# Performance work log

Measured on AMD Instinct MI355X. Metric: run time of the kernel, lower is better.

The kernel has to match this reference:

```python
import jax, jax.numpy as jnp
import numpy as np

N = 38332        # nodes = poi_len - 1 (pinned by fc_layer in_features)
POI_LEN = 38333
CAT_LEN = 400
POI_DIM = 300
CAT_DIM = 100
C = 128          # gcn_channel
L = 5            # gcn_layers
E = 1200000      # edges
NEG = 0.01       # nn.LeakyReLU default slope
GAT_NEG = 0.2    # GATConv attention slope


def _leaky(x, s=NEG):
    return jnp.where(x > 0, x, s * x)


def _gcn_conv(x, W, b, src, dst, ew):
    # PyG GCNConv: self-loops already appended in (src,dst,ew); symmetric norm
    xw = x @ W
    deg = jax.ops.segment_sum(ew, dst, num_segments=N)
    dinv = jnp.where(deg > 0, jax.lax.rsqrt(deg), 0.0)
    norm = dinv[src] * ew * dinv[dst]
    out = jax.ops.segment_sum(xw[src] * norm[:, None], dst, num_segments=N)
    return out + b


def _gat_conv(x, W, a_src, a_dst, b, src, dst):
    # PyG GATConv, 1 head; self-loops already in (src,dst)
    xw = x @ W                      # [N, C]
    al = xw @ a_src                 # [N]
    ar = xw @ a_dst                 # [N]
    e = _leaky(al[src] + ar[dst], GAT_NEG)          # [E+N]
    emax = jax.ops.segment_max(e, dst, num_segments=N)
    ex = jnp.exp(e - emax[dst])
    denom = jax.ops.segment_sum(ex, dst, num_segments=N)
    att = ex / denom[dst]
    out = jax.ops.segment_sum(xw[src] * att[:, None], dst, num_segments=N)
    return out + b


def _graph_norm(x, gamma, beta, alpha, eps=1e-5):
    # PyG GraphNorm over the single graph (all nodes)
    mean = x.mean(0)
    xc = x - alpha * mean
    var = (xc * xc).mean(0)
    return gamma * xc * jax.lax.rsqrt(var + eps) + beta


def _forward(poi_ids, cat_ids, feat3, edge_index, edge_weight, poi_emb, cat_emb,
             Win, b_in, gcn_W, gcn_b, gn_gamma, gn_beta, gn_alpha,
             gat_W, gat_asrc, gat_adst, gat_b, Wout, b_out,
             fc_W1, fc_b1, fc_W2, fc_b2):
    loops = jnp.arange(N, dtype=edge_index.dtype)
    src = jnp.concatenate([edge_index[0], loops])
    dst = jnp.concatenate([edge_index[1], loops])
    ew = jnp.concatenate([edge_weight, jnp.ones((N,), edge_weight.dtype)])
    # node features: [poi_emb | cat_emb | 3 raw floats] -> [N, 403]
    feat = jnp.concatenate([poi_emb[poi_ids], cat_emb[cat_ids], feat3], axis=1)
    x = _leaky(_gcn_conv(feat, Win, b_in, src, dst, ew))
    for l in range(L):  # GcnUnit stack (shared GraphNorm within a unit)
        t = _leaky(_graph_norm(_gcn_conv(x, gcn_W[l], gcn_b[l], src, dst, ew),
                               gn_gamma[l], gn_beta[l], gn_alpha[l]))
        x = x + t
        t = _leaky(_graph_norm(_gat_conv(x, gat_W[l], gat_asrc[l], gat_adst[l], gat_b[l], src, dst),
                               gn_gamma[l], gn_beta[l], gn_alpha[l]))
        x = x + t
    x = _leaky(_gcn_conv(x, Wout, b_out, src, dst, ew)).reshape(-1)  # [N]
    h = jax.nn.relu(x @ fc_W1 + fc_b1)
    return jax.nn.relu(h @ fc_W2 + fc_b2)  # [POI_LEN]


def setup_inputs() -> dict:
    key = jax.random.key(0)
    ks = iter(jax.random.split(key, 24))
    nrm = lambda s, sc=0.05: jax.random.normal(next(ks), s, dtype=jnp.float32) * sc
    return {
        'poi_ids': jax.random.randint(next(ks), (N,), 0, POI_LEN),
        'cat_ids': jax.random.randint(next(ks), (N,), 0, CAT_LEN),
        'feat3': jax.random.normal(next(ks), (N, 3), dtype=jnp.float32),
        'edge_index': jax.random.randint(next(ks), (2, E), 0, N),
        'edge_weight': jax.random.uniform(next(ks), (E,), dtype=jnp.float32),
        'poi_emb': nrm((POI_LEN, POI_DIM)),
        'cat_emb': nrm((CAT_LEN, CAT_DIM)),
        'Win': nrm((POI_DIM + CAT_DIM + 3, C)),
        'b_in': jnp.zeros((C,), jnp.float32),
        'gcn_W': nrm((L, C, C)),
        'gcn_b': jnp.zeros((L, C), jnp.float32),
        'gn_gamma': jnp.ones((L, C), jnp.float32),
        'gn_beta': jnp.zeros((L, C), jnp.float32),
        'gn_alpha': jnp.ones((L, C), jnp.float32),
        'gat_W': nrm((L, C, C)),
        'gat_asrc': nrm((L, C)),
        'gat_adst': nrm((L, C)),
        'gat_b': jnp.zeros((L, C), jnp.float32),
        'Wout': nrm((C, 1)),
        'b_out': jnp.zeros((1,), jnp.float32),
        'fc_W1': nrm((N, 128)),
        'fc_b1': jnp.zeros((128,), jnp.float32),
        'fc_W2': nrm((128, POI_LEN)),
        'fc_b2': jnp.zeros((POI_LEN,), jnp.float32),
    }


def reference(poi_ids, cat_ids, feat3, edge_index, edge_weight, poi_emb, cat_emb,
              Win, b_in, gcn_W, gcn_b, gn_gamma, gn_beta, gn_alpha,
              gat_W, gat_asrc, gat_adst, gat_b, Wout, b_out,
              fc_W1, fc_b1, fc_W2, fc_b2):
    return _forward(poi_ids, cat_ids, feat3, edge_index, edge_weight, poi_emb, cat_emb,
                    Win, b_in, gcn_W, gcn_b, gn_gamma, gn_beta, gn_alpha,
                    gat_W, gat_asrc, gat_adst, gat_b, Wout, b_out,
                    fc_W1, fc_b1, fc_W2, fc_b2)
```

## Files before the change

### kernel.cpp

```cpp
#include <hip/hip_runtime.h>

typedef unsigned short ushort_t;
typedef __attribute__((ext_vector_type(8))) short short8v;
typedef __attribute__((ext_vector_type(4))) float floatx4;

__device__ __forceinline__ float b2f(ushort_t u) {
    unsigned int x = ((unsigned int)u) << 16;
    float f; __builtin_memcpy(&f, &x, 4); return f;
}
__device__ __forceinline__ ushort_t f2b(float f) {
    unsigned int x; __builtin_memcpy(&x, &f, 4);
    unsigned int lsb = (x >> 16) & 1u;
    x += 0x7fffu + lsb;
    return (ushort_t)(x >> 16);
}
__device__ __forceinline__ float leaky01(float v) { return v > 0.f ? v : 0.01f * v; }

__global__ void init_k(int* cnt, int N) {
    int i = blockIdx.x * 256 + threadIdx.x;
    if (i < N) cnt[i] = 1;
}

__global__ void count_k(const int* __restrict__ ei, int* cnt, int E) {
    int e = blockIdx.x * 256 + threadIdx.x;
    if (e < E) atomicAdd(&cnt[ei[E + e]], 1);
}

__launch_bounds__(1024)
__global__ void scan_k(const int* __restrict__ cnt, int* rp, int n) {
    __shared__ int wsum[16];
    int tid = threadIdx.x; int lane = tid & 63, wid = tid >> 6;
    int base = 0;
    for (int start = 0; start < n; start += 4096) {
        int v[4]; int s = 0;
        #pragma unroll
        for (int j = 0; j < 4; ++j) {
            int i = start + tid * 4 + j;
            v[j] = (i < n) ? cnt[i] : 0; s += v[j];
        }
        int sc = s;
        #pragma unroll
        for (int off = 1; off < 64; off <<= 1) {
            int t = __shfl_up(sc, off);
            if (lane >= off) sc += t;
        }
        if (lane == 63) wsum[wid] = sc;
        __syncthreads();
        if (wid == 0) {
            int ws = (lane < 16) ? wsum[lane] : 0;
            #pragma unroll
            for (int off = 1; off < 16; off <<= 1) {
                int t = __shfl_up(ws, off);
                if (lane >= off) ws += t;
            }
            if (lane < 16) wsum[lane] = ws;
        }
        __syncthreads();
        int wbase = (wid > 0) ? wsum[wid - 1] : 0;
        int excl = base + wbase + (sc - s);
        #pragma unroll
        for (int j = 0; j < 4; ++j) {
            int i = start + tid * 4 + j;
            if (i < n) rp[i] = excl;
            excl += v[j];
        }
        int total = wsum[15];
        __syncthreads();
        base += total;
    }
    if (tid == 0) rp[n] = base;
}

__global__ void post_k(const int* __restrict__ rp, int* fill, float2* er, int N) {
    int i = blockIdx.x * 256 + threadIdx.x;
    if (i < N) {
        int p = rp[i];
        fill[i] = p + 1;
        er[p] = make_float2(__int_as_float(i), 1.0f);
    }
}

__global__ void scat_k(const int* __restrict__ ei, const float* __restrict__ ew,
                       int* fill, float2* er, int E) {
    int e = blockIdx.x * 256 + threadIdx.x;
    if (e < E) {
        int dst = ei[E + e];
        int pos = atomicAdd(&fill[dst], 1);
        er[pos] = make_float2(__int_as_float(ei[e]), ew[e]);
    }
}

__global__ void deg_k(const int* __restrict__ rp, const float2* __restrict__ er,
                      float* dinv, int N) {
    int wave = threadIdx.x >> 6, lane = threadIdx.x & 63;
    int node = blockIdx.x * 4 + wave;
    if (node >= N) return;
    int s0 = rp[node], end = rp[node + 1];
    float sum = 0.f;
    for (int s = s0 + lane; s < end; s += 64) sum += er[s].y;
    #pragma unroll
    for (int off = 32; off; off >>= 1) sum += __shfl_xor(sum, off);
    if (lane == 0) dinv[node] = rsqrtf(sum);
}

__global__ void coef_k(const int* __restrict__ rp, float2* er,
                       const float* __restrict__ dinv, int N) {
    int wave = threadIdx.x >> 6, lane = threadIdx.x & 63;
    int node = blockIdx.x * 4 + wave;
    if (node >= N) return;
    int s0 = rp[node], end = rp[node + 1];
    float di = dinv[node];
    for (int s = s0 + lane; s < end; s += 64) {
        float2 r = er[s];
        int src = __float_as_int(r.x);
        r.y = dinv[src] * r.y * di;
        er[s] = r;
    }
}

__global__ void prep_w(const float* __restrict__ gcn_W, const float* __restrict__ gat_W,
                       const float* __restrict__ Win, ushort_t* __restrict__ wt,
                       ushort_t* __restrict__ wtin) {
    int idx = blockIdx.x * 256 + threadIdx.x;
    if (idx < 10 * 16384) {
        int l = idx >> 14, r = idx & 16383;
        int n = r >> 7, k = r & 127;
        const float* src = (l < 5) ? (gcn_W + l * 16384) : (gat_W + (l - 5) * 16384);
        wt[idx] = f2b(src[k * 128 + n]);
    } else {
        int idx2 = idx - 10 * 16384;
        if (idx2 < 128 * 320) {
            int n = idx2 / 320, k = idx2 - n * 320;
            wtin[idx2] = f2b(k < 300 ? Win[k * 128 + n] : 0.f);
        }
    }
}

__global__ void cat_proj_k(const float* __restrict__ ce, const float* __restrict__ Win,
                           float* __restrict__ cp) {
    __shared__ float row[100];
    int r = blockIdx.x, tid = threadIdx.x;
    if (tid < 100) row[tid] = ce[r * 100 + tid];
    __syncthreads();
    float acc = 0.f;
    #pragma unroll 4
    for (int k = 0; k < 100; ++k) acc += row[k] * Win[(300 + k) * 128 + tid];
    cp[r * 128 + tid] = acc;
}

__launch_bounds__(256)
__global__ void poi_gemm(const float* __restrict__ pe, const ushort_t* __restrict__ wtin,
                         ushort_t* __restrict__ pp, int P) {
    __shared__ __align__(16) ushort_t As[64 * 328];
    int tid = threadIdx.x;
    int wid = tid >> 6, lane = tid & 63;
    int r0 = blockIdx.x * 64;
    #pragma unroll
    for (int p = 0; p < 80; ++p) {
        int idx = tid + p * 256;
        int row = idx / 320, k = idx - row * 320;
        float v = 0.f;
        if (k < 300 && (r0 + row) < P) v = pe[(size_t)(r0 + row) * 300 + k];
        As[row * 328 + k] = f2b(v);
    }
    __syncthreads();
    int m = lane & 15, q = lane >> 4;
    short8v af[10];
    #pragma unroll
    for (int kc = 0; kc < 10; ++kc)
        af[kc] = *(const short8v*)&As[(wid * 16 + m) * 328 + kc * 32 + q * 8];
    #pragma unroll
    for (int ct = 0; ct < 8; ++ct) {
        const ushort_t* wr = wtin + (size_t)(ct * 16 + m) * 320 + q * 8;
        floatx4 acc = {0.f, 0.f, 0.f, 0.f};
        #pragma unroll
        for (int kc = 0; kc < 10; ++kc) {
            short8v b = *(const short8v*)(wr + kc * 32);
            acc = __builtin_amdgcn_mfma_f32_16x16x32_bf16(af[kc], b, acc, 0, 0, 0);
        }
        int col = ct * 16 + m;
        #pragma unroll
        for (int rg = 0; rg < 4; ++rg) {
            int row = r0 + wid * 16 + q * 4 + rg;
            if (row < P) pp[(size_t)row * 128 + col] = f2b(acc[rg]);
        }
    }
}

__launch_bounds__(256)
__global__ void gemm_mfma(const ushort_t* __restrict__ xb, const ushort_t* __restrict__ wt,
                          ushort_t* __restrict__ xw, int N) {
    __shared__ __align__(16) ushort_t As[64 * 136];
    int tid = threadIdx.x;
    int wid = tid >> 6, lane = tid & 63;
    int r0 = blockIdx.x * 64;
    #pragma unroll
    for (int p = 0; p < 4; ++p) {
        int idx = tid + p * 256;
        int row = idx >> 4, c8 = idx & 15;
        short8v v = *(const short8v*)&xb[(size_t)(r0 + row) * 128 + c8 * 8];
        *(short8v*)&As[row * 136 + c8 * 8] = v;
    }
    __syncthreads();
    int m = lane & 15, q = lane >> 4;
    const int ar = (wid * 16 + m) * 136 + q * 8;
    short8v a0 = *(const short8v*)&As[ar];
    short8v a1 = *(const short8v*)&As[ar + 32];
    short8v a2 = *(const short8v*)&As[ar + 64];
    short8v a3 = *(const short8v*)&As[ar + 96];
    #pragma unroll
    for (int ct = 0; ct < 8; ++ct) {
        const ushort_t* wr = wt + (size_t)(ct * 16 + m) * 128 + q * 8;
        short8v b0 = *(const short8v*)(wr);
        short8v b1 = *(const short8v*)(wr + 32);
        short8v b2 = *(const short8v*)(wr + 64);
        short8v b3 = *(const short8v*)(wr + 96);
        floatx4 acc = {0.f, 0.f, 0.f, 0.f};
        acc = __builtin_amdgcn_mfma_f32_16x16x32_bf16(a0, b0, acc, 0, 0, 0);
        acc = __builtin_amdgcn_mfma_f32_16x16x32_bf16(a1, b1, acc, 0, 0, 0);
        acc = __builtin_amdgcn_mfma_f32_16x16x32_bf16(a2, b2, acc, 0, 0, 0);
        acc = __builtin_amdgcn_mfma_f32_16x16x32_bf16(a3, b3, acc, 0, 0, 0);
        int col = ct * 16 + m;
        #pragma unroll
        for (int rg = 0; rg < 4; ++rg) {
            int row = r0 + wid * 16 + q * 4 + rg;
            if (row < N) xw[(size_t)row * 128 + col] = f2b(acc[rg]);
        }
    }
}

__global__ void combine_k(const ushort_t* __restrict__ pp, const float* __restrict__ cp,
                          const int* __restrict__ poi_ids, const int* __restrict__ cat_ids,
                          const float* __restrict__ feat3, const float* __restrict__ Win,
                          ushort_t* __restrict__ xw, int N) {
    __shared__ float wf0[128], wf1[128], wf2[128];
    int tid = threadIdx.x;
    if (tid < 128) {
        wf0[tid] = Win[400 * 128 + tid];
        wf1[tid] = Win[401 * 128 + tid];
        wf2[tid] = Win[402 * 128 + tid];
    }
    __syncthreads();
    int node = blockIdx.x * 2 + (tid >> 7);
    int c = tid & 127;
    if (node >= N) return;
    int pid = poi_ids[node], cid = cat_ids[node];
    float f0 = feat3[node * 3], f1 = feat3[node * 3 + 1], f2 = feat3[node * 3 + 2];
    float v = b2f(pp[(size_t)pid * 128 + c]) + cp[cid * 128 + c]
            + f0 * wf0[c] + f1 * wf1[c] + f2 * wf2[c];
    xw[(size_t)node * 128 + c] = f2b(v);
}

template <int MODE>
__launch_bounds__(256)
__global__ void agg_k(const ushort_t* __restrict__ xw, const int* __restrict__ rp,
                      const float2* __restrict__ er,
                      const float* __restrict__ al, const float* __restrict__ ar,
                      const float* __restrict__ bias, float* __restrict__ g,
                      ushort_t* __restrict__ xb, int N) {
    int wave = threadIdx.x >> 6, lane = threadIdx.x & 63;
    int node = blockIdx.x * 4 + wave;
    if (node >= N) return;
    int s0 = __builtin_amdgcn_readfirstlane(rp[node]);
    int end = __builtin_amdgcn_readfirstlane(rp[node + 1]);
    float mmax = 0.f, inv = 0.f, ari = 0.f;
    if (MODE == 2) {
        ari = ar[node];
        float mm = -1e30f;
        for (int s = s0 + lane; s < end; s += 64) {
            int src = __float_as_int(er[s].x);
            float e = al[src] + ari; e = e > 0.f ? e : 0.2f * e;
            mm = fmaxf(mm, e);
        }
        #pragma unroll
        for (int off = 32; off; off >>= 1) mm = fmaxf(mm, __shfl_xor(mm, off));
        float ds = 0.f;
        for (int s = s0 + lane; s < end; s += 64) {
            int src = __float_as_int(er[s].x);
            float e = al[src] + ari; e = e > 0.f ? e : 0.2f * e;
            ds += __expf(e - mm);
        }
        #pragma unroll
        for (int off = 32; off; off >>= 1) ds += __shfl_xor(ds, off);
        mmax = mm;
        inv = 1.f / ds;
    }
    int c = lane * 2;
    float ax = 0.f, ay = 0.f;
    int s = s0;
    for (; s + 8 <= end; s += 8) {
        float2 r[8]; ushort2 u[8]; float cf[8];
        #pragma unroll
        for (int j = 0; j < 8; ++j) r[j] = er[s + j];
        #pragma unroll
        for (int j = 0; j < 8; ++j) {
            int src = __float_as_int(r[j].x);
            u[j] = *(const ushort2*)&xw[(size_t)src * 128 + c];
            if (MODE == 2) {
                float e = al[src] + ari; e = e > 0.f ? e : 0.2f * e;
                cf[j] = __expf(e - mmax) * inv;
            } else cf[j] = r[j].y;
        }
        #pragma unroll
        for (int j = 0; j < 8; ++j) {
            ax += cf[j] * b2f(u[j].x);
            ay += cf[j] * b2f(u[j].y);
        }
    }
    for (; s < end; ++s) {
        float2 r = er[s];
        int src = __float_as_int(r.x);
        float cf;
        if (MODE == 2) {
            float e = al[src] + ari; e = e > 0.f ? e : 0.2f * e;
            cf = __expf(e - mmax) * inv;
        } else cf = r.y;
        ushort2 u = *(const ushort2*)&xw[(size_t)src * 128 + c];
        ax += cf * b2f(u.x);
        ay += cf * b2f(u.y);
    }
    float2 b = *(const float2*)&bias[c];
    ax += b.x; ay += b.y;
    if (MODE == 1) {
        ax = leaky01(ax); ay = leaky01(ay);
        float2 o; o.x = ax; o.y = ay;
        *(float2*)&g[(size_t)node * 128 + c] = o;
        ushort2 ub; ub.x = f2b(ax); ub.y = f2b(ay);
        *(ushort2*)&xb[(size_t)node * 128 + c] = ub;
    } else {
        float2 o; o.x = ax; o.y = ay;
        *(float2*)&g[(size_t)node * 128 + c] = o;
    }
}

__global__ void moments_k(const float* __restrict__ g, float* mom, int n32) {
    __shared__ float s1s[256][4], s2s[256][4];
    int tid = threadIdx.x;
    long long T = (long long)gridDim.x * 256;
    float a1[4] = {0.f, 0.f, 0.f, 0.f}, a2[4] = {0.f, 0.f, 0.f, 0.f};
    const float4* g4 = (const float4*)g;
    for (long long idx = (long long)blockIdx.x * 256 + tid; idx < n32; idx += T) {
        float4 v = g4[idx];
        a1[0] += v.x; a2[0] += v.x * v.x;
        a1[1] += v.y; a2[1] += v.y * v.y;
        a1[2] += v.z; a2[2] += v.z * v.z;
        a1[3] += v.w; a2[3] += v.w * v.w;
    }
    #pragma unroll
    for (int j = 0; j < 4; ++j) { s1s[tid][j] = a1[j]; s2s[tid][j] = a2[j]; }
    __syncthreads();
    if (tid < 32) {
        float r1[4] = {0.f, 0.f, 0.f, 0.f}, r2[4] = {0.f, 0.f, 0.f, 0.f};
        for (int t = tid; t < 256; t += 32) {
            #pragma unroll
            for (int j = 0; j < 4; ++j) { r1[j] += s1s[t][j]; r2[j] += s2s[t][j]; }
        }
        #pragma unroll
        for (int j = 0; j < 4; ++j) {
            atomicAdd(&mom[4 * tid + j], r1[j]);
            atomicAdd(&mom[128 + 4 * tid + j], r2[j]);
        }
    }
}

__global__ void normresid_k(float* __restrict__ x, const float* __restrict__ g,
                            const float* __restrict__ mom,
                            const float* __restrict__ gamma, const float* __restrict__ beta,
                            const float* __restrict__ alpha, ushort_t* __restrict__ xb,
                            int n32, int N) {
    __shared__ float sc[128], sh[128];
    int tid = threadIdx.x;
    if (tid < 128) {
        float m = mom[tid] / (float)N;
        float a = alpha[tid];
        float var = mom[128 + tid] / (float)N - 2.f * a * m * m + a * a * m * m;
        float s = gamma[tid] * rsqrtf(var + 1e-5f);
        sc[tid] = s;
        sh[tid] = beta[tid] - s * a * m;
    }
    __syncthreads();
    const float4* g4 = (const float4*)g;
    float4* x4 = (float4*)x;
    ushort4* xb4 = (ushort4*)xb;
    for (long long idx = (long long)blockIdx.x * 256 + tid; idx < n32;
         idx += (long long)gridDim.x * 256) {
        int c0 = (int)((idx * 4) & 127);
        float4 gv = g4[idx];
        float4 xv = x4[idx];
        xv.x += leaky01(sc[c0] * gv.x + sh[c0]);
        xv.y += leaky01(sc[c0 + 1] * gv.y + sh[c0 + 1]);
        xv.z += leaky01(sc[c0 + 2] * gv.z + sh[c0 + 2]);
        xv.w += leaky01(sc[c0 + 3] * gv.w + sh[c0 + 3]);
        x4[idx] = xv;
        ushort4 ub;
        ub.x = f2b(xv.x); ub.y = f2b(xv.y); ub.z = f2b(xv.z); ub.w = f2b(xv.w);
        xb4[idx] = ub;
    }
}

__global__ void alar_k(const ushort_t* __restrict__ xw, const float* __restrict__ asrc,
                       const float* __restrict__ adst, float* al, float* ar, int N) {
    __shared__ float ls[128], ld[128];
    int tid = threadIdx.x;
    if (tid < 128) { ls[tid] = asrc[tid]; ld[tid] = adst[tid]; }
    __syncthreads();
    int i = blockIdx.x * 256 + tid;
    if (i >= N) return;
    const ushort_t* row = xw + (size_t)i * 128;
    float a = 0.f, b = 0.f;
    #pragma unroll 4
    for (int c = 0; c < 128; c += 4) {
        ushort4 u = *(const ushort4*)(row + c);
        float f0 = b2f(u.x), f1 = b2f(u.y), f2 = b2f(u.z), f3 = b2f(u.w);
        a += f0 * ls[c] + f1 * ls[c + 1] + f2 * ls[c + 2] + f3 * ls[c + 3];
        b += f0 * ld[c] + f1 * ld[c + 1] + f2 * ld[c + 2] + f3 * ld[c + 3];
    }
    al[i] = a; ar[i] = b;
}

__global__ void ydot_k(const float* __restrict__ x, const float* __restrict__ Wout,
                       float* yv, int N) {
    __shared__ float w[128];
    int tid = threadIdx.x;
    if (tid < 128) w[tid] = Wout[tid];
    __syncthreads();
    int i = blockIdx.x * 256 + tid;
    if (i >= N) return;
    const float* row = x + (size_t)i * 128;
    float acc = 0.f;
    #pragma unroll 4
    for (int c = 0; c < 128; c += 4) {
        float4 v = *(const float4*)(row + c);
        acc += v.x * w[c] + v.y * w[c + 1] + v.z * w[c + 2] + v.w * w[c + 3];
    }
    yv[i] = acc;
}

__global__ void aggs_k(const float* __restrict__ yv, const int* __restrict__ rp,
                       const float2* __restrict__ er,
                       const float* __restrict__ b_out, float* xs, int N) {
    int wave = threadIdx.x >> 6, lane = threadIdx.x & 63;
    int node = blockIdx.x * 4 + wave;
    if (node >= N) return;
    int s0 = rp[node], end = rp[node + 1];
    float acc = 0.f;
    for (int s = s0 + lane; s < end; s += 64) {
        float2 r = er[s];
        acc += r.y * yv[__float_as_int(r.x)];
    }
    #pragma unroll
    for (int off = 32; off; off >>= 1) acc += __shfl_xor(acc, off);
    if (lane == 0) xs[node] = leaky01(acc + b_out[0]);
}

__global__ void fc1_k(const float* __restrict__ xs, const float* __restrict__ W1,
                      float* hacc, int N) {
    __shared__ float sd[256];
    int tid = threadIdx.x;
    int j = tid & 127, half = tid >> 7;
    int r0 = blockIdx.x * 256;
    float acc = 0.f;
    for (int rr = half; rr < 256; rr += 2) {
        int r = r0 + rr;
        if (r < N) acc += xs[r] * W1[(size_t)r * 128 + j];
    }
    sd[tid] = acc;
    __syncthreads();
    if (tid < 128) atomicAdd(&hacc[tid], sd[tid] + sd[tid + 128]);
}

__global__ void fc2_k(const float* __restrict__ hacc, const float* __restrict__ b1,
                      const float* __restrict__ W2, const float* __restrict__ b2v,
                      float* out, int P) {
    __shared__ float hs[128];
    int tid = threadIdx.x;
    if (tid < 128) {
        float h = hacc[tid] + b1[tid];
        hs[tid] = h > 0.f ? h : 0.f;
    }
    __syncthreads();
    int p = blockIdx.x * 256 + tid;
    if (p >= P) return;
    float acc = 0.f;
    #pragma unroll 8
    for (int j = 0; j < 128; ++j) acc += hs[j] * W2[(size_t)j * P + p];
    acc += b2v[p];
    out[p] = acc > 0.f ? acc : 0.f;
}

extern "C" void kernel_launch(void* const* d_in, const int* in_sizes, int n_in,
                              void* d_out, int out_size, void* d_ws, size_t ws_size,
                              hipStream_t stream) {
    const int*   poi_ids  = (const int*)d_in[0];
    const int*   cat_ids  = (const int*)d_in[1];
    const float* feat3    = (const float*)d_in[2];
    const int*   ei       = (const int*)d_in[3];
    const float* ew       = (const float*)d_in[4];
    const float* poi_emb  = (const float*)d_in[5];
    const float* cat_emb  = (const float*)d_in[6];
    const float* Win      = (const float*)d_in[7];
    const float* b_in     = (const float*)d_in[8];
    const float* gcn_W    = (const float*)d_in[9];
    const float* gcn_b    = (const float*)d_in[10];
    const float* gn_gamma = (const float*)d_in[11];
    const float* gn_beta  = (const float*)d_in[12];
    const float* gn_alpha = (const float*)d_in[13];
    const float* gat_W    = (const float*)d_in[14];
    const float* gat_asrc = (const float*)d_in[15];
    const float* gat_adst = (const float*)d_in[16];
    const float* gat_b    = (const float*)d_in[17];
    const float* Wout     = (const float*)d_in[18];
    const float* b_out    = (const float*)d_in[19];
    const float* fc_W1    = (const float*)d_in[20];
    const float* fc_b1    = (const float*)d_in[21];
    const float* fc_W2    = (const float*)d_in[22];
    const float* fc_b2    = (const float*)d_in[23];

    const int N = in_sizes[0];
    const int E = in_sizes[4];
    const int POI = in_sizes[5] / 300;
    const int P = out_size;
    const int TOT = E + N;
    const int n128 = N * 128;
    const int n32 = n128 / 4;
    const int NPAD = ((N + 63) / 64) * 64;
    const int PPAD = ((POI + 63) / 64) * 64;

    char* w = (char*)d_ws;
    size_t off = 0;
    auto take = [&](size_t bytes) -> char* {
        char* p = w + off;
        off = (off + bytes + 255) & ~(size_t)255;
        return p;
    };
    float*    x    = (float*)take((size_t)n128 * 4);
    float*    g    = (float*)take((size_t)n128 * 4);
    ushort_t* xb   = (ushort_t*)take((size_t)NPAD * 128 * 2);
    ushort_t* xw   = (ushort_t*)take((size_t)NPAD * 128 * 2);
    ushort_t* pp   = (ushort_t*)take((size_t)PPAD * 128 * 2);
    float*    cp   = (float*)take((size_t)400 * 128 * 4);
    ushort_t* wt   = (ushort_t*)take((size_t)10 * 16384 * 2);
    ushort_t* wtin = (ushort_t*)take((size_t)128 * 320 * 2);
    int*    rp   = (int*)take((size_t)(N + 1) * 4);
    int*    cnt  = (int*)take((size_t)N * 4);
    int*    fill = (int*)take((size_t)N * 4);
    float*  dinv = (float*)take((size_t)N * 4);
    float2* er   = (float2*)take((size_t)TOT * 8);
    float*  al   = (float*)take((size_t)N * 4);
    float*  ar   = (float*)take((size_t)N * 4);
    float*  yv   = (float*)take((size_t)N * 4);
    float*  xs   = (float*)take((size_t)N * 4);
    float*  mom  = (float*)take((size_t)(10 * 256 + 128) * 4);
    float*  hacc = mom + 10 * 256;

    const int gN    = (N + 255) / 256;
    const int gE    = (E + 255) / 256;
    const int gMM   = NPAD / 64;
    const int gPOI  = PPAD / 64;
    const int gW    = (N + 3) / 4;
    const int gP    = (P + 255) / 256;

    hipMemsetAsync(mom, 0, (size_t)(10 * 256 + 128) * 4, stream);

    init_k<<<gN, 256, 0, stream>>>(cnt, N);
    count_k<<<gE, 256, 0, stream>>>(ei, cnt, E);
    scan_k<<<1, 1024, 0, stream>>>(cnt, rp, N);
    post_k<<<gN, 256, 0, stream>>>(rp, fill, er, N);
    scat_k<<<gE, 256, 0, stream>>>(ei, ew, fill, er, E);
    deg_k<<<gW, 256, 0, stream>>>(rp, er, dinv, N);
    coef_k<<<gW, 256, 0, stream>>>(rp, er, dinv, N);

    prep_w<<<(10 * 16384 + 128 * 320 + 255) / 256, 256, 0, stream>>>(gcn_W, gat_W, Win, wt, wtin);
    cat_proj_k<<<400, 128, 0, stream>>>(cat_emb, Win, cp);
    poi_gemm<<<gPOI, 256, 0, stream>>>(poi_emb, wtin, pp, POI);
    combine_k<<<(N + 1) / 2, 256, 0, stream>>>(pp, cp, poi_ids, cat_ids, feat3, Win, xw, N);
    agg_k<1><<<gW, 256, 0, stream>>>(xw, rp, er, nullptr, nullptr, b_in, x, xb, N);

    for (int l = 0; l < 5; ++l) {
        gemm_mfma<<<gMM, 256, 0, stream>>>(xb, wt + (size_t)l * 16384, xw, N);
        agg_k<0><<<gW, 256, 0, stream>>>(xw, rp, er, nullptr, nullptr, gcn_b + l * 128, g, nullptr, N);
        moments_k<<<240, 256, 0, stream>>>(g, mom + (2 * l) * 256, n32);
        normresid_k<<<1024, 256, 0, stream>>>(x, g, mom + (2 * l) * 256,
                                              gn_gamma + l * 128, gn_beta + l * 128,
                                              gn_alpha + l * 128, xb, n32, N);
        gemm_mfma<<<gMM, 256, 0, stream>>>(xb, wt + (size_t)(5 + l) * 16384, xw, N);
        alar_k<<<gN, 256, 0, stream>>>(xw, gat_asrc + l * 128, gat_adst + l * 128, al, ar, N);
        agg_k<2><<<gW, 256, 0, stream>>>(xw, rp, er, al, ar, gat_b + l * 128, g, nullptr, N);
        moments_k<<<240, 256, 0, stream>>>(g, mom + (2 * l + 1) * 256, n32);
        normresid_k<<<1024, 256, 0, stream>>>(x, g, mom + (2 * l + 1) * 256,
                                              gn_gamma + l * 128, gn_beta + l * 128,
                                              gn_alpha + l * 128, xb, n32, N);
    }

    ydot_k<<<gN, 256, 0, stream>>>(x, Wout, yv, N);
    aggs_k<<<gW, 256, 0, stream>>>(yv, rp, er, b_out, xs, N);

    fc1_k<<<(N + 255) / 256, 256, 0, stream>>>(xs, fc_W1, hacc, N);
    fc2_k<<<gP, 256, 0, stream>>>(hacc, fc_b1, fc_W2, fc_b2, (float*)d_out, P);
}
```

Measured before the change: 1.581 ms.

## Fuse GraphNorm residual into GEMM, fuse alar into GEMM, restructure aggregation

GraphNorm+residual+bf16 conversion now runs in the GEMM prologue and the attention logits al/ar are computed in the GEMM epilogue, which removes the separate normresid, alar and ydot kernels and the xb buffer. Edge normalization coefficients are computed on the fly from dinv instead of in a coef_k pass. CSR build uses the atomic return position instead of a second atomic fill. Aggregation switches to 8-channel vector loads with 4 edges processed in parallel per wave, followed by cross-lane reductions. The trade-off is extra dinv gathers per edge and a heavier GEMM prologue.

```diff
diff --git a/kernel.cpp b/kernel.cpp
--- a/kernel.cpp
+++ b/kernel.cpp
@@ -21,9 +21,9 @@
     if (i < N) cnt[i] = 1;
 }
 
-__global__ void count_k(const int* __restrict__ ei, int* cnt, int E) {
+__global__ void count_k(const int* __restrict__ ei, int* cnt, int* pos, int E) {
     int e = blockIdx.x * 256 + threadIdx.x;
-    if (e < E) atomicAdd(&cnt[ei[E + e]], 1);
+    if (e < E) pos[e] = atomicAdd(&cnt[ei[E + e]], 1);
 }
 
 __launch_bounds__(1024)
@@ -71,22 +71,18 @@
     if (tid == 0) rp[n] = base;
 }
 
-__global__ void post_k(const int* __restrict__ rp, int* fill, float2* er, int N) {
+__global__ void post_k(const int* __restrict__ rp, float2* er, int N) {
     int i = blockIdx.x * 256 + threadIdx.x;
-    if (i < N) {
-        int p = rp[i];
-        fill[i] = p + 1;
-        er[p] = make_float2(__int_as_float(i), 1.0f);
-    }
+    if (i < N) er[rp[i]] = make_float2(__int_as_float(i), 1.0f);
 }
 
 __global__ void scat_k(const int* __restrict__ ei, const float* __restrict__ ew,
-                       int* fill, float2* er, int E) {
+                       const int* __restrict__ rp, const int* __restrict__ pos,
+                       float2* er, int E) {
     int e = blockIdx.x * 256 + threadIdx.x;
     if (e < E) {
         int dst = ei[E + e];
-        int pos = atomicAdd(&fill[dst], 1);
-        er[pos] = make_float2(__int_as_float(ei[e]), ew[e]);
+        er[rp[dst] + pos[e]] = make_float2(__int_as_float(ei[e]), ew[e]);
     }
 }
 
@@ -101,21 +97,6 @@
     #pragma unroll
     for (int off = 32; off; off >>= 1) sum += __shfl_xor(sum, off);
     if (lane == 0) dinv[node] = rsqrtf(sum);
-}
-
-__global__ void coef_k(const int* __restrict__ rp, float2* er,
-                       const float* __restrict__ dinv, int N) {
-    int wave = threadIdx.x >> 6, lane = threadIdx.x & 63;
-    int node = blockIdx.x * 4 + wave;
-    if (node >= N) return;
-    int s0 = rp[node], end = rp[node + 1];
-    float di = dinv[node];
-    for (int s = s0 + lane; s < end; s += 64) {
-        float2 r = er[s];
-        int src = __float_as_int(r.x);
-        r.y = dinv[src] * r.y * di;
-        er[s] = r;
-    }
 }
 
 __global__ void prep_w(const float* __restrict__ gcn_W, const float* __restrict__ gat_W,
@@ -187,27 +168,61 @@
     }
 }
 
+template <int NORM, int ALAR>
 __launch_bounds__(256)
-__global__ void gemm_mfma(const ushort_t* __restrict__ xb, const ushort_t* __restrict__ wt,
-                          ushort_t* __restrict__ xw, int N) {
+__global__ void gemm_fused(float* __restrict__ x, const float* __restrict__ gsrc,
+                           const float* __restrict__ mom,
+                           const float* __restrict__ gamma, const float* __restrict__ beta,
+                           const float* __restrict__ alpha,
+                           const ushort_t* __restrict__ wt,
+                           const float* __restrict__ asrc, const float* __restrict__ adst,
+                           ushort_t* __restrict__ xw,
+                           float* __restrict__ al, float* __restrict__ ar, int N) {
     __shared__ __align__(16) ushort_t As[64 * 136];
+    __shared__ float sc[128], sh[128];
     int tid = threadIdx.x;
+    if (NORM) {
+        if (tid < 128) {
+            float mmean = mom[tid] / (float)N;
+            float a = alpha[tid];
+            float var = mom[128 + tid] / (float)N - 2.f * a * mmean * mmean + a * a * mmean * mmean;
+            float s = gamma[tid] * rsqrtf(var + 1e-5f);
+            sc[tid] = s;
+            sh[tid] = beta[tid] - s * a * mmean;
+        }
+        __syncthreads();
+    }
+    int r0 = blockIdx.x * 64;
+    #pragma unroll
+    for (int p = 0; p < 8; ++p) {
+        int idx = tid + p * 256;
+        int row = idx >> 5, c4 = (idx & 31) * 4;
+        int grow = r0 + row;
+        float4 xv = make_float4(0.f, 0.f, 0.f, 0.f);
+        if (grow < N) {
+            xv = *(const float4*)&x[(size_t)grow * 128 + c4];
+            if (NORM) {
+                float4 gv = *(const float4*)&gsrc[(size_t)grow * 128 + c4];
+                xv.x += leaky01(sc[c4] * gv.x + sh[c4]);
+                xv.y += leaky01(sc[c4 + 1] * gv.y + sh[c4 + 1]);
+                xv.z += leaky01(sc[c4 + 2] * gv.z + sh[c4 + 2]);
+                xv.w += leaky01(sc[c4 + 3] * gv.w + sh[c4 + 3]);
+                *(float4*)&x[(size_t)grow * 128 + c4] = xv;
+            }
+        }
+        ushort4 b;
+        b.x = f2b(xv.x); b.y = f2b(xv.y); b.z = f2b(xv.z); b.w = f2b(xv.w);
+        *(ushort4*)&As[row * 136 + c4] = b;
+    }
+    __syncthreads();
     int wid = tid >> 6, lane = tid & 63;
-    int r0 = blockIdx.x * 64;
-    #pragma unroll
-    for (int p = 0; p < 4; ++p) {
-        int idx = tid + p * 256;
-        int row = idx >> 4, c8 = idx & 15;
-        short8v v = *(const short8v*)&xb[(size_t)(r0 + row) * 128 + c8 * 8];
-        *(short8v*)&As[row * 136 + c8 * 8] = v;
-    }
-    __syncthreads();
     int m = lane & 15, q = lane >> 4;
-    const int ar = (wid * 16 + m) * 136 + q * 8;
-    short8v a0 = *(const short8v*)&As[ar];
-    short8v a1 = *(const short8v*)&As[ar + 32];
-    short8v a2 = *(const short8v*)&As[ar + 64];
-    short8v a3 = *(const short8v*)&As[ar + 96];
+    const int arr = (wid * 16 + m) * 136 + q * 8;
+    short8v a0 = *(const short8v*)&As[arr];
+    short8v a1 = *(const short8v*)&As[arr + 32];
+    short8v a2 = *(const short8v*)&As[arr + 64];
+    short8v a3 = *(const short8v*)&As[arr + 96];
+    float alsum[4] = {0.f, 0.f, 0.f, 0.f}, arsum[4] = {0.f, 0.f, 0.f, 0.f};
     #pragma unroll
     for (int ct = 0; ct < 8; ++ct) {
         const ushort_t* wr = wt + (size_t)(ct * 16 + m) * 128 + q * 8;
@@ -221,10 +236,35 @@
         acc = __builtin_amdgcn_mfma_f32_16x16x32_bf16(a2, b2, acc, 0, 0, 0);
         acc = __builtin_amdgcn_mfma_f32_16x16x32_bf16(a3, b3, acc, 0, 0, 0);
         int col = ct * 16 + m;
+        if (ALAR) {
+            float av = asrc[col], dv = adst[col];
+            #pragma unroll
+            for (int rg = 0; rg < 4; ++rg) {
+                alsum[rg] += acc[rg] * av;
+                arsum[rg] += acc[rg] * dv;
+            }
+        }
         #pragma unroll
         for (int rg = 0; rg < 4; ++rg) {
             int row = r0 + wid * 16 + q * 4 + rg;
             if (row < N) xw[(size_t)row * 128 + col] = f2b(acc[rg]);
+        }
+    }
+    if (ALAR) {
+        #pragma unroll
+        for (int rg = 0; rg < 4; ++rg) {
+            #pragma unroll
+            for (int off = 1; off < 16; off <<= 1) {
+                alsum[rg] += __shfl_xor(alsum[rg], off);
+                arsum[rg] += __shfl_xor(arsum[rg], off);
+            }
+        }
+        if (m == 0) {
+            #pragma unroll
+            for (int rg = 0; rg < 4; ++rg) {
+                int row = r0 + wid * 16 + q * 4 + rg;
+                if (row < N) { al[row] = alsum[rg]; ar[row] = arsum[rg]; }
+            }
         }
     }
 }
@@ -254,16 +294,17 @@
 template <int MODE>
 __launch_bounds__(256)
 __global__ void agg_k(const ushort_t* __restrict__ xw, const int* __restrict__ rp,
-                      const float2* __restrict__ er,
+                      const float2* __restrict__ er, const float* __restrict__ dinv,
                       const float* __restrict__ al, const float* __restrict__ ar,
-                      const float* __restrict__ bias, float* __restrict__ g,
-                      ushort_t* __restrict__ xb, int N) {
+                      const float* __restrict__ bias, float* __restrict__ g, int N) {
     int wave = threadIdx.x >> 6, lane = threadIdx.x & 63;
     int node = blockIdx.x * 4 + wave;
     if (node >= N) return;
     int s0 = __builtin_amdgcn_readfirstlane(rp[node]);
     int end = __builtin_amdgcn_readfirstlane(rp[node + 1]);
-    float mmax = 0.f, inv = 0.f, ari = 0.f;
+    int g8 = lane >> 4;
+    int c8 = (lane & 15) * 8;
+    float dn = 0.f, mmax = 0.f, inv = 0.f, ari = 0.f;
     if (MODE == 2) {
         ari = ar[node];
         float mm = -1e30f;
@@ -284,52 +325,44 @@
         for (int off = 32; off; off >>= 1) ds += __shfl_xor(ds, off);
         mmax = mm;
         inv = 1.f / ds;
-    }
-    int c = lane * 2;
-    float ax = 0.f, ay = 0.f;
-    int s = s0;
-    for (; s + 8 <= end; s += 8) {
-        float2 r[8]; ushort2 u[8]; float cf[8];
-        #pragma unroll
-        for (int j = 0; j < 8; ++j) r[j] = er[s + j];
-        #pragma unroll
-        for (int j = 0; j < 8; ++j) {
-            int src = __float_as_int(r[j].x);
-            u[j] = *(const ushort2*)&xw[(size_t)src * 128 + c];
-            if (MODE == 2) {
-                float e = al[src] + ari; e = e > 0.f ? e : 0.2f * e;
-                cf[j] = __expf(e - mmax) * inv;
-            } else cf[j] = r[j].y;
-        }
-        #pragma unroll
-        for (int j = 0; j < 8; ++j) {
-            ax += cf[j] * b2f(u[j].x);
-            ay += cf[j] * b2f(u[j].y);
-        }
-    }
-    for (; s < end; ++s) {
-        float2 r = er[s];
+    } else {
+        dn = dinv[node];
+    }
+    float acc[8] = {0.f, 0.f, 0.f, 0.f, 0.f, 0.f, 0.f, 0.f};
+    auto body = [&](int e) {
+        float2 r = er[e];
         int src = __float_as_int(r.x);
         float cf;
         if (MODE == 2) {
-            float e = al[src] + ari; e = e > 0.f ? e : 0.2f * e;
-            cf = __expf(e - mmax) * inv;
-        } else cf = r.y;
-        ushort2 u = *(const ushort2*)&xw[(size_t)src * 128 + c];
-        ax += cf * b2f(u.x);
-        ay += cf * b2f(u.y);
-    }
-    float2 b = *(const float2*)&bias[c];
-    ax += b.x; ay += b.y;
-    if (MODE == 1) {
-        ax = leaky01(ax); ay = leaky01(ay);
-        float2 o; o.x = ax; o.y = ay;
-        *(float2*)&g[(size_t)node * 128 + c] = o;
-        ushort2 ub; ub.x = f2b(ax); ub.y = f2b(ay);
-        *(ushort2*)&xb[(size_t)node * 128 + c] = ub;
-    } else {
-        float2 o; o.x = ax; o.y = ay;
-        *(float2*)&g[(size_t)node * 128 + c] = o;
+            float ev = al[src] + ari; ev = ev > 0.f ? ev : 0.2f * ev;
+            cf = __expf(ev - mmax) * inv;
+        } else {
+            cf = dinv[src] * r.y * dn;
+        }
+        const short8v u = *(const short8v*)&xw[(size_t)src * 128 + c8];
+        #pragma unroll
+        for (int k = 0; k < 8; ++k) acc[k] += cf * b2f((ushort_t)u[k]);
+    };
+    int e = s0 + g8;
+    for (; e + 12 < end; e += 16) { body(e); body(e + 4); body(e + 8); body(e + 12); }
+    for (; e < end; e += 4) body(e);
+    #pragma unroll
+    for (int k = 0; k < 8; ++k) {
+        acc[k] += __shfl_xor(acc[k], 16);
+        acc[k] += __shfl_xor(acc[k], 32);
+    }
+    if (g8 == 0) {
+        float4 o1, o2;
+        o1.x = acc[0] + bias[c8];     o1.y = acc[1] + bias[c8 + 1];
+        o1.z = acc[2] + bias[c8 + 2]; o1.w = acc[3] + bias[c8 + 3];
+        o2.x = acc[4] + bias[c8 + 4]; o2.y = acc[5] + bias[c8 + 5];
+        o2.z = acc[6] + bias[c8 + 6]; o2.w = acc[7] + bias[c8 + 7];
+        if (MODE == 1) {
+            o1.x = leaky01(o1.x); o1.y = leaky01(o1.y); o1.z = leaky01(o1.z); o1.w = leaky01(o1.w);
+            o2.x = leaky01(o2.x); o2.y = leaky01(o2.y); o2.z = leaky01(o2.z); o2.w = leaky01(o2.w);
+        }
+        *(float4*)&g[(size_t)node * 128 + c8] = o1;
+        *(float4*)&g[(size_t)node * 128 + c8 + 4] = o2;
     }
 }
 
@@ -363,12 +396,12 @@
     }
 }
 
-__global__ void normresid_k(float* __restrict__ x, const float* __restrict__ g,
+__global__ void norm_ydot_k(const float* __restrict__ x, const float* __restrict__ g,
                             const float* __restrict__ mom,
                             const float* __restrict__ gamma, const float* __restrict__ beta,
-                            const float* __restrict__ alpha, ushort_t* __restrict__ xb,
-                            int n32, int N) {
-    __shared__ float sc[128], sh[128];
+                            const float* __restrict__ alpha, const float* __restrict__ Wout,
+                            float* __restrict__ yv, int N) {
+    __shared__ float sc[128], sh[128], wv[128];
     int tid = threadIdx.x;
     if (tid < 128) {
         float m = mom[tid] / (float)N;
@@ -377,76 +410,36 @@
         float s = gamma[tid] * rsqrtf(var + 1e-5f);
         sc[tid] = s;
         sh[tid] = beta[tid] - s * a * m;
-    }
-    __syncthreads();
-    const float4* g4 = (const float4*)g;
-    float4* x4 = (float4*)x;
-    ushort4* xb4 = (ushort4*)xb;
-    for (long long idx = (long long)blockIdx.x * 256 + tid; idx < n32;
-         idx += (long long)gridDim.x * 256) {
-        int c0 = (int)((idx * 4) & 127);
-        float4 gv = g4[idx];
-        float4 xv = x4[idx];
-        xv.x += leaky01(sc[c0] * gv.x + sh[c0]);
-        xv.y += leaky01(sc[c0 + 1] * gv.y + sh[c0 + 1]);
-        xv.z += leaky01(sc[c0 + 2] * gv.z + sh[c0 + 2]);
-        xv.w += leaky01(sc[c0 + 3] * gv.w + sh[c0 + 3]);
-        x4[idx] = xv;
-        ushort4 ub;
-        ub.x = f2b(xv.x); ub.y = f2b(xv.y); ub.z = f2b(xv.z); ub.w = f2b(xv.w);
-        xb4[idx] = ub;
-    }
-}
-
-__global__ void alar_k(const ushort_t* __restrict__ xw, const float* __restrict__ asrc,
-                       const float* __restrict__ adst, float* al, float* ar, int N) {
-    __shared__ float ls[128], ld[128];
-    int tid = threadIdx.x;
-    if (tid < 128) { ls[tid] = asrc[tid]; ld[tid] = adst[tid]; }
-    __syncthreads();
-    int i = blockIdx.x * 256 + tid;
-    if (i >= N) return;
-    const ushort_t* row = xw + (size_t)i * 128;
-    float a = 0.f, b = 0.f;
-    #pragma unroll 4
-    for (int c = 0; c < 128; c += 4) {
-        ushort4 u = *(const ushort4*)(row + c);
-        float f0 = b2f(u.x), f1 = b2f(u.y), f2 = b2f(u.z), f3 = b2f(u.w);
-        a += f0 * ls[c] + f1 * ls[c + 1] + f2 * ls[c + 2] + f3 * ls[c + 3];
-        b += f0 * ld[c] + f1 * ld[c + 1] + f2 * ld[c + 2] + f3 * ld[c + 3];
-    }
-    al[i] = a; ar[i] = b;
-}
-
-__global__ void ydot_k(const float* __restrict__ x, const float* __restrict__ Wout,
-                       float* yv, int N) {
-    __shared__ float w[128];
-    int tid = threadIdx.x;
-    if (tid < 128) w[tid] = Wout[tid];
-    __syncthreads();
-    int i = blockIdx.x * 256 + tid;
-    if (i >= N) return;
-    const float* row = x + (size_t)i * 128;
-    float acc = 0.f;
-    #pragma unroll 4
-    for (int c = 0; c < 128; c += 4) {
-        float4 v = *(const float4*)(row + c);
-        acc += v.x * w[c] + v.y * w[c + 1] + v.z * w[c + 2] + v.w * w[c + 3];
-    }
-    yv[i] = acc;
+        wv[tid] = Wout[tid];
+    }
+    __syncthreads();
+    int wave = tid >> 6, lane = tid & 63;
+    int node = blockIdx.x * 4 + wave;
+    if (node >= N) return;
+    int c = lane * 2;
+    float2 gv = *(const float2*)&g[(size_t)node * 128 + c];
+    float2 xv = *(const float2*)&x[(size_t)node * 128 + c];
+    float v0 = xv.x + leaky01(sc[c] * gv.x + sh[c]);
+    float v1 = xv.y + leaky01(sc[c + 1] * gv.y + sh[c + 1]);
+    float acc = v0 * wv[c] + v1 * wv[c + 1];
+    #pragma unroll
+    for (int off = 32; off; off >>= 1) acc += __shfl_xor(acc, off);
+    if (lane == 0) yv[node] = acc;
 }
 
 __global__ void aggs_k(const float* __restrict__ yv, const int* __restrict__ rp,
-                       const float2* __restrict__ er,
+                       const float2* __restrict__ er, const float* __restrict__ dinv,
                        const float* __restrict__ b_out, float* xs, int N) {
     int wave = threadIdx.x >> 6, lane = threadIdx.x & 63;
     int node = blockIdx.x * 4 + wave;
     if (node >= N) return;
     int s0 = rp[node], end = rp[node + 1];
+    float dn = dinv[node];
     float acc = 0.f;
     for (int s = s0 + lane; s < end; s += 64) {
         float2 r = er[s];
-        acc += r.y * yv[__float_as_int(r.x)];
+        int src = __float_as_int(r.x);
+        acc += dinv[src] * r.y * dn * yv[src];
     }
     #pragma unroll
     for (int off = 32; off; off >>= 1) acc += __shfl_xor(acc, off);
@@ -535,7 +528,6 @@
     };
     float*    x    = (float*)take((size_t)n128 * 4);
     float*    g    = (float*)take((size_t)n128 * 4);
-    ushort_t* xb   = (ushort_t*)take((size_t)NPAD * 128 * 2);
     ushort_t* xw   = (ushort_t*)take((size_t)NPAD * 128 * 2);
     ushort_t* pp   = (ushort_t*)take((size_t)PPAD * 128 * 2);
     float*    cp   = (float*)take((size_t)400 * 128 * 4);
@@ -543,7 +535,7 @@
     ushort_t* wtin = (ushort_t*)take((size_t)128 * 320 * 2);
     int*    rp   = (int*)take((size_t)(N + 1) * 4);
     int*    cnt  = (int*)take((size_t)N * 4);
-    int*    fill = (int*)take((size_t)N * 4);
+    int*    pos  = (int*)take((size_t)E * 4);
     float*  dinv = (float*)take((size_t)N * 4);
     float2* er   = (float2*)take((size_t)TOT * 8);
     float*  al   = (float*)take((size_t)N * 4);
@@ -553,47 +545,57 @@
     float*  mom  = (float*)take((size_t)(10 * 256 + 128) * 4);
     float*  hacc = mom + 10 * 256;
 
-    const int gN    = (N + 255) / 256;
-    const int gE    = (E + 255) / 256;
-    const int gMM   = NPAD / 64;
-    const int gPOI  = PPAD / 64;
-    const int gW    = (N + 3) / 4;
-    const int gP    = (P + 255) / 256;
+    const int gN   = (N + 255) / 256;
+    const int gE   = (E + 255) / 256;
+    const int gMM  = NPAD / 64;
+    const int gPOI = PPAD / 64;
+    const int gW   = (N + 3) / 4;
+    const int gP   = (P + 255) / 256;
 
     hipMemsetAsync(mom, 0, (size_t)(10 * 256 + 128) * 4, stream);
 
     init_k<<<gN, 256, 0, stream>>>(cnt, N);
-    count_k<<<gE, 256, 0, stream>>>(ei, cnt, E);
+    count_k<<<gE, 256, 0, stream>>>(ei, cnt, pos, E);
     scan_k<<<1, 1024, 0, stream>>>(cnt, rp, N);
-    post_k<<<gN, 256, 0, stream>>>(rp, fill, er, N);
-    scat_k<<<gE, 256, 0, stream>>>(ei, ew, fill, er, E);
+    post_k<<<gN, 256, 0, stream>>>(rp, er, N);
+    scat_k<<<gE, 256, 0, stream>>>(ei, ew, rp, pos, er, E);
     deg_k<<<gW, 256, 0, stream>>>(rp, er, dinv, N);
-    coef_k<<<gW, 256, 0, stream>>>(rp, er, dinv, N);
 
     prep_w<<<(10 * 16384 + 128 * 320 + 255) / 256, 256, 0, stream>>>(gcn_W, gat_W, Win, wt, wtin);
     cat_proj_k<<<400, 128, 0, stream>>>(cat_emb, Win, cp);
     poi_gemm<<<gPOI, 256, 0, stream>>>(poi_emb, wtin, pp, POI);
     combine_k<<<(N + 1) / 2, 256, 0, stream>>>(pp, cp, poi_ids, cat_ids, feat3, Win, xw, N);
-    agg_k<1><<<gW, 256, 0, stream>>>(xw, rp, er, nullptr, nullptr, b_in, x, xb, N);
+    agg_k<1><<<gW, 256, 0, stream>>>(xw, rp, er, dinv, nullptr, nullptr, b_in, x, N);
 
     for (int l = 0; l < 5; ++l) {
-        gemm_mfma<<<gMM, 256, 0, stream>>>(xb, wt + (size_t)l * 16384, xw, N);
-        agg_k<0><<<gW, 256, 0, stream>>>(xw, rp, er, nullptr, nullptr, gcn_b + l * 128, g, nullptr, N);
+        if (l == 0)
+            gemm_fused<0, 0><<<gMM, 256, 0, stream>>>(x, nullptr, nullptr, nullptr, nullptr,
+                                                      nullptr, wt, nullptr, nullptr,
+                                                      xw, nullptr, nullptr, N);
+        else
+            gemm_fused<1, 0><<<gMM, 256, 0, stream>>>(x, g, mom + (2 * l - 1) * 256,
+                                                      gn_gamma + (l - 1) * 128,
+                                                      gn_beta + (l - 1) * 128,
+                                                      gn_alpha + (l - 1) * 128,
+                                                      wt + (size_t)l * 16384, nullptr, nullptr,
+                                                      xw, nullptr, nullptr, N);
+        agg_k<0><<<gW, 256, 0, stream>>>(xw, rp, er, dinv, nullptr, nullptr,
+                                         gcn_b + l * 128, g, N);
         moments_k<<<240, 256, 0, stream>>>(g, mom + (2 * l) * 256, n32);
-        normresid_k<<<1024, 256, 0, stream>>>(x, g, mom + (2 * l) * 256,
-                                              gn_gamma + l * 128, gn_beta + l * 128,
-                                              gn_alpha + l * 128, xb, n32, N);
-        gemm_mfma<<<gMM, 256, 0, stream>>>(xb, wt + (size_t)(5 + l) * 16384, xw, N);
-        alar_k<<<gN, 256, 0, stream>>>(xw, gat_asrc + l * 128, gat_adst + l * 128, al, ar, N);
-        agg_k<2><<<gW, 256, 0, stream>>>(xw, rp, er, al, ar, gat_b + l * 128, g, nullptr, N);
+
+        gemm_fused<1, 1><<<gMM, 256, 0, stream>>>(x, g, mom + (2 * l) * 256,
+                                                  gn_gamma + l * 128, gn_beta + l * 128,
+                                                  gn_alpha + l * 128,
+                                                  wt + (size_t)(5 + l) * 16384,
+                                                  gat_asrc + l * 128, gat_adst + l * 128,
+                                                  xw, al, ar, N);
+        agg_k<2><<<gW, 256, 0, stream>>>(xw, rp, er, nullptr, al, ar, gat_b + l * 128, g, N);
         moments_k<<<240, 256, 0, stream>>>(g, mom + (2 * l + 1) * 256, n32);
-        normresid_k<<<1024, 256, 0, stream>>>(x, g, mom + (2 * l + 1) * 256,
-                                              gn_gamma + l * 128, gn_beta + l * 128,
-                                              gn_alpha + l * 128, xb, n32, N);
-    }
-
-    ydot_k<<<gN, 256, 0, stream>>>(x, Wout, yv, N);
-    aggs_k<<<gW, 256, 0, stream>>>(yv, rp, er, b_out, xs, N);
+    }
+
+    norm_ydot_k<<<gW, 256, 0, stream>>>(x, g, mom + 9 * 256, gn_gamma + 4 * 128,
+                                        gn_beta + 4 * 128, gn_alpha + 4 * 128, Wout, yv, N);
+    aggs_k<<<gW, 256, 0, stream>>>(yv, rp, er, dinv, b_out, xs, N);
 
     fc1_k<<<(N + 255) / 256, 256, 0, stream>>>(xs, fc_W1, hacc, N);
     fc2_k<<<gP, 256, 0, stream>>>(hacc, fc_b1, fc_W2, fc_b2, (float*)d_out, P);
```

Measured after the change: 1.454 ms. -8.0%, faster.
